# Kernel optimization log

Hardware: AMD Instinct MI355X
Metric: run time of the kernel (lower is better)

Reference implementation:

```python
import jax, jax.numpy as jnp
import numpy as np

H, D = 8, 32
IN, HID, OUT = 256, 256, 128
N_PAR, N_FIG, N_TAB, N_CIT = 100000, 20000, 20000, 50000
E = 200000


def setup_inputs() -> dict:
    key = jax.random.key(0)
    ks = iter(jax.random.split(key, 80))
    def nrm(shape, s=0.05):
        return jax.random.normal(next(ks), shape, dtype=jnp.float32) * s
    def ridx(n):
        return jax.random.randint(next(ks), (E,), 0, n, dtype=jnp.int32)
    inp = {
        'x_par': nrm((N_PAR, IN), 1.0), 'x_fig': nrm((N_FIG, IN), 1.0),
        'x_tab': nrm((N_TAB, IN), 1.0), 'x_cit': nrm((N_CIT, IN), 1.0),
    }
    for t in ['par', 'fig', 'tab', 'cit']:
        inp[f'Wp_{t}'] = nrm((IN, HID)); inp[f'bp_{t}'] = nrm((HID,))
    for et in ['pf', 'fp', 'pt', 'tp', 'pc', 'cp']:
        inp[f'a_{et}_s'] = nrm((H, D)); inp[f'a_{et}_d'] = nrm((H, D))
    inp['k_w'] = nrm((HID, HID)); inp['k_b'] = nrm((HID,)); inp['q'] = nrm((HID,))
    for t in ['par', 'fig', 'tab', 'cit']:
        inp[f'Wh_{t}'] = nrm((HID, OUT)); inp[f'bh_{t}'] = nrm((OUT,))
    inp['cls_w'] = nrm((2 * OUT, 1)); inp['cls_b'] = nrm((1,))
    inp['pf_src'] = ridx(N_PAR); inp['pf_dst'] = ridx(N_FIG)
    inp['fp_src'] = ridx(N_FIG); inp['fp_dst'] = ridx(N_PAR)
    inp['pt_src'] = ridx(N_PAR); inp['pt_dst'] = ridx(N_TAB)
    inp['tp_src'] = ridx(N_TAB); inp['tp_dst'] = ridx(N_PAR)
    inp['pc_src'] = ridx(N_PAR); inp['pc_dst'] = ridx(N_CIT)
    inp['cp_src'] = ridx(N_CIT); inp['cp_dst'] = ridx(N_PAR)
    inp['target_node_idx'] = 5
    return inp


def _agg(xs, xd, si, di, a_s, a_d, n_dst):
    # HANConv metapath aggregation: GAT-style attention + per-dst softmax + scatter-sum + relu
    as_ = jnp.einsum('nhd,hd->nh', xs, a_s)            # [Ns,H]
    ad_ = jnp.einsum('nhd,hd->nh', xd, a_d)            # [Nd,H]
    alpha = jax.nn.leaky_relu(as_[si] + ad_[di], 0.2)  # [E,H]
    m = jax.ops.segment_max(alpha, di, num_segments=n_dst)
    m = jnp.where(jnp.isfinite(m), m, 0.0)
    ex = jnp.exp(alpha - m[di])
    den = jax.ops.segment_sum(ex, di, num_segments=n_dst)
    w = ex / (den[di] + 1e-16)
    out = jax.ops.segment_sum(xs[si] * w[:, :, None], di, num_segments=n_dst)  # [Nd,H,D]
    return jax.nn.relu(out.reshape(n_dst, H * D))


def _group(outs, q, kw, kb):
    # HANConv semantic (metapath-level) attention
    st = jnp.stack(outs)                               # [M,N,F]
    kmean = jnp.tanh(st @ kw + kb).mean(axis=1)        # [M,F]
    attn = jax.nn.softmax(kmean @ q)                   # [M]
    return jnp.einsum('m,mnf->nf', attn, st)


def reference(x_par, x_fig, x_tab, x_cit,
              Wp_par, bp_par, Wp_fig, bp_fig, Wp_tab, bp_tab, Wp_cit, bp_cit,
              a_pf_s, a_pf_d, a_fp_s, a_fp_d, a_pt_s, a_pt_d,
              a_tp_s, a_tp_d, a_pc_s, a_pc_d, a_cp_s, a_cp_d,
              k_w, k_b, q,
              Wh_par, bh_par, Wh_fig, bh_fig, Wh_tab, bh_tab, Wh_cit, bh_cit,
              cls_w, cls_b,
              pf_src, pf_dst, fp_src, fp_dst, pt_src, pt_dst,
              tp_src, tp_dst, pc_src, pc_dst, cp_src, cp_dst,
              target_node_idx):
    # per-node-type input projection
    h_par = (x_par @ Wp_par + bp_par).reshape(-1, H, D)
    h_fig = (x_fig @ Wp_fig + bp_fig).reshape(-1, H, D)
    h_tab = (x_tab @ Wp_tab + bp_tab).reshape(-1, H, D)
    h_cit = (x_cit @ Wp_cit + bp_cit).reshape(-1, H, D)
    # per-metapath message passing, grouped per destination node type
    o_fig = _group([_agg(h_par, h_fig, pf_src, pf_dst, a_pf_s, a_pf_d, N_FIG)], q, k_w, k_b)
    o_tab = _group([_agg(h_par, h_tab, pt_src, pt_dst, a_pt_s, a_pt_d, N_TAB)], q, k_w, k_b)
    o_cit = _group([_agg(h_par, h_cit, pc_src, pc_dst, a_pc_s, a_pc_d, N_CIT)], q, k_w, k_b)
    o_par = _group([
        _agg(h_fig, h_par, fp_src, fp_dst, a_fp_s, a_fp_d, N_PAR),
        _agg(h_tab, h_par, tp_src, tp_dst, a_tp_s, a_tp_d, N_PAR),
        _agg(h_cit, h_par, cp_src, cp_dst, a_cp_s, a_cp_d, N_PAR),
    ], q, k_w, k_b)
    # output heads (table/cited_paper heads computed in the original but unused for scores)
    par_emb = o_par @ Wh_par + bh_par
    fig_emb = o_fig @ Wh_fig + bh_fig
    _ = o_tab @ Wh_tab + bh_tab
    _ = o_cit @ Wh_cit + bh_cit
    # pairwise classifier: target figure embedding broadcast against every paragraph
    target = fig_emb[target_node_idx]
    comb = jnp.concatenate(
        [jnp.broadcast_to(target[None, :], (par_emb.shape[0], OUT)), par_emb], axis=1)
    scores = (comb @ cls_w + cls_b)[:, 0]
    return scores
```

## Files before the change

### kernel.cpp

```cpp
#include <hip/hip_runtime.h>
#include <hip/hip_bf16.h>
#include <math.h>

typedef float f32x4 __attribute__((ext_vector_type(4)));
typedef short bf16x8 __attribute__((ext_vector_type(8)));

#define NPAR 100000
#define NFIG 20000
#define NTAB 20000
#define NCIT 50000
#define NEDGE 200000
#define CAP 32
#define PFCAP 79

__device__ __forceinline__ unsigned short f2b(float f) {
    union { float f; unsigned u; } x; x.f = f;
    unsigned r = x.u + 0x7FFFu + ((x.u >> 16) & 1u);
    return (unsigned short)(r >> 16);
}
__device__ __forceinline__ float b2f(unsigned short b) {
    union { unsigned u; float f; } x; x.u = ((unsigned)b) << 16; return x.f;
}
__device__ __forceinline__ float fast_tanh(float x) {
    float e = __expf(2.f * x);
    return 1.f - 2.f * __builtin_amdgcn_rcpf(e + 1.f);
}
__device__ __forceinline__ void async_copy16(const unsigned short* g, unsigned short* l) {
    __builtin_amdgcn_global_load_lds(
        (const __attribute__((address_space(1))) unsigned int*)g,
        (__attribute__((address_space(3))) unsigned int*)l, 16, 0, 0);
}

__global__ void k_transpose5(const float* __restrict__ W0, const float* __restrict__ W1,
                             const float* __restrict__ W2, const float* __restrict__ W3,
                             const float* __restrict__ W4, unsigned short* __restrict__ WT) {
    int b = blockIdx.x, which = b >> 8, k = b & 255, n = threadIdx.x;
    const float* W = which == 0 ? W0 : which == 1 ? W1 : which == 2 ? W2 : which == 3 ? W3 : W4;
    WT[(size_t)which * 65536 + n * 256 + k] = f2b(W[k * 256 + n]);
}

__global__ void k_precompute(const float* __restrict__ WhF, const float* __restrict__ bhF,
                             const float* __restrict__ WhP, const float* __restrict__ bhP,
                             const float* __restrict__ clsw, const float* __restrict__ clsb,
                             float* __restrict__ u, float* __restrict__ v, float* __restrict__ smallb) {
    int t = threadIdx.x;
    float su = 0.f, sv = 0.f;
    for (int j = 0; j < 128; ++j) {
        su += WhF[t * 128 + j] * clsw[j];
        sv += WhP[t * 128 + j] * clsw[128 + j];
    }
    u[t] = su; v[t] = sv;
    if (t == 0) {
        float c = clsb[0];
        for (int j = 0; j < 128; ++j) c += bhF[j] * clsw[j] + bhP[j] * clsw[128 + j];
        smallb[264] = c;
    }
}

__global__ void k_edges(const int* __restrict__ d0, const int* __restrict__ d1,
                        const int* __restrict__ d2, int* __restrict__ count,
                        int* __restrict__ elist,
                        const int* __restrict__ psrc, const int* __restrict__ pdst,
                        const int* __restrict__ tgtp, int* __restrict__ mlist) {
    int b = blockIdx.x;
    int m = b / 782;
    int e = (b - m * 782) * 256 + threadIdx.x;
    if (e >= NEDGE) return;
    if (m < 3) {
        const int* dst = m == 0 ? d0 : m == 1 ? d1 : d2;
        int d = dst[e];
        int* cnt = count + (size_t)m * NPAR;
        int* el = elist + (size_t)m * NPAR * CAP;
        int slot = atomicAdd(&cnt[d], 1);
        if (slot < CAP) el[(size_t)d * CAP + slot] = e;
    } else {
        if (pdst[e] == tgtp[0]) {
            int slot = atomicAdd(&mlist[0], 1);
            if (slot < PFCAP) mlist[1 + slot] = psrc[e];
        }
    }
}

struct ProjPack {
    const float* X[4];
    const unsigned short* WT[4];
    const float* bias[4];
    unsigned short* H[4];
    const float* av[16];
    float* ov[16];
    int nrows[4];
    int bbase[4];
    int nv[4];
};

#define LOADA(k0, A0, A1) do { \
    const float4* _p = reinterpret_cast<const float4*>(Arow + (k0)); \
    A0 = _p[0]; A1 = _p[1]; } while (0)
#define WRITEA(buf, A0, A1) do { \
    __align__(16) unsigned short _t[8]; \
    _t[0] = f2b(A0.x); _t[1] = f2b(A0.y); _t[2] = f2b(A0.z); _t[3] = f2b(A0.w); \
    _t[4] = f2b(A1.x); _t[5] = f2b(A1.y); _t[6] = f2b(A1.z); _t[7] = f2b(A1.w); \
    *reinterpret_cast<uint4*>(&As[buf][arow * 32 + acol]) = *reinterpret_cast<const uint4*>(_t); } while (0)

__global__ __launch_bounds__(512, 4) void k_gemm_proj(ProjPack p) {
    __shared__ __align__(16) unsigned short As[2][128 * 32];
    __shared__ __align__(16) unsigned short Bs[2][256 * 32];
    int bid = blockIdx.x;
    int ty = (bid >= p.bbase[1]) + (bid >= p.bbase[2]) + (bid >= p.bbase[3]);
    int m0 = (bid - p.bbase[ty]) * 128;
    const float* Xf = p.X[ty];
    const unsigned short* B = p.WT[ty];
    unsigned short* Hout = p.H[ty];
    int Nrows = p.nrows[ty];
    int nv = p.nv[ty];

    int t = threadIdx.x, l = t & 63, w = t >> 6;
    int wm = (w >> 2) * 64, wn = (w & 3) * 64;
    int lr = l & 15, hi = l >> 4;
    int arow = t >> 2, acol = (t & 3) * 8;
    int arow_c = m0 + arow; if (arow_c > Nrows - 1) arow_c = Nrows - 1;
    const float* Arow = Xf + (size_t)arow_c * 256 + acol;
    f32x4 acc[4][4] = {};
    float4 aP0, aP1, aQ0, aQ1;

    auto stageB = [&](int buf, int k0) {
#pragma unroll
        for (int i = 0; i < 2; ++i) {
            int rowb = w * 32 + i * 16;
            async_copy16(B + (size_t)(rowb + (l >> 2)) * 256 + k0 + (l & 3) * 8,
                         &Bs[buf][rowb * 32]);
        }
    };

    LOADA(0, aP0, aP1);
    stageB(0, 0);
    WRITEA(0, aP0, aP1);
    LOADA(32, aQ0, aQ1);
    asm volatile("s_waitcnt vmcnt(2) lgkmcnt(0)" ::: "memory");
    __builtin_amdgcn_s_barrier();

#pragma unroll
    for (int ks = 0; ks < 8; ++ks) {
        int cur = ks & 1;
        if (ks < 7) stageB(cur ^ 1, (ks + 1) * 32);
        if (ks < 6) {
            if ((ks & 1) == 0) LOADA((ks + 2) * 32, aP0, aP1);
            else               LOADA((ks + 2) * 32, aQ0, aQ1);
        }
        bf16x8 af[4], bfr[4];
#pragma unroll
        for (int mm = 0; mm < 4; ++mm)
            af[mm] = *reinterpret_cast<const bf16x8*>(&As[cur][(wm + mm * 16 + lr) * 32 + hi * 8]);
#pragma unroll
        for (int nn = 0; nn < 4; ++nn)
            bfr[nn] = *reinterpret_cast<const bf16x8*>(&Bs[cur][(wn + nn * 16 + lr) * 32 + hi * 8]);
#pragma unroll
        for (int mm = 0; mm < 4; ++mm)
#pragma unroll
            for (int nn = 0; nn < 4; ++nn)
                acc[mm][nn] = __builtin_amdgcn_mfma_f32_16x16x32_bf16(bfr[nn], af[mm], acc[mm][nn], 0, 0, 0);
        if (ks < 7) {
            if ((ks & 1) == 0) WRITEA(cur ^ 1, aQ0, aQ1);
            else               WRITEA(cur ^ 1, aP0, aP1);
            if (ks < 6) asm volatile("s_waitcnt vmcnt(2) lgkmcnt(0)" ::: "memory");
            else        asm volatile("s_waitcnt vmcnt(0) lgkmcnt(0)" ::: "memory");
            __builtin_amdgcn_s_barrier();
        }
    }

    __syncthreads();
    float* sattp = (float*)&As[0][0];
    unsigned short* Hst = &Bs[0][0];

    float4 bv4[4], av4[4][4];
#pragma unroll
    for (int nn = 0; nn < 4; ++nn)
        bv4[nn] = *reinterpret_cast<const float4*>(p.bias[ty] + wn + nn * 16 + hi * 4);
#pragma unroll
    for (int v = 0; v < 4; ++v)
        if (v < nv) {
            const float* A = p.av[ty * 4 + v];
#pragma unroll
            for (int nn = 0; nn < 4; ++nn)
                av4[v][nn] = *reinterpret_cast<const float4*>(A + wn + nn * 16 + hi * 4);
        }
    int h0 = (w & 3) * 2;
#pragma unroll
    for (int mm = 0; mm < 4; ++mm) {
        int lrow = wm + mm * 16 + lr;
        float sv[4][2] = {};
#pragma unroll
        for (int nn = 0; nn < 4; ++nn) {
            float c0 = acc[mm][nn][0] + bv4[nn].x;
            float c1 = acc[mm][nn][1] + bv4[nn].y;
            float c2 = acc[mm][nn][2] + bv4[nn].z;
            float c3 = acc[mm][nn][3] + bv4[nn].w;
#pragma unroll
            for (int v = 0; v < 4; ++v)
                if (v < nv)
                    sv[v][nn >> 1] += c0 * av4[v][nn].x + c1 * av4[v][nn].y +
                                      c2 * av4[v][nn].z + c3 * av4[v][nn].w;
        }
#pragma unroll
        for (int v = 0; v < 4; ++v)
            if (v < nv) {
#pragma unroll
                for (int hp = 0; hp < 2; ++hp) {
                    float s = sv[v][hp];
                    s += __shfl_xor(s, 16); s += __shfl_xor(s, 32);
                    if (hi == 0) sattp[v * 1024 + lrow * 8 + h0 + hp] = s;
                }
            }
    }

    if (ty != 0) {
        for (int hf = 0; hf < 2; ++hf) {
            if ((w >> 2) == hf) {
#pragma unroll
                for (int mm = 0; mm < 4; ++mm) {
                    int lr2 = mm * 16 + lr;
                    int swz = (lr2 & 7) << 4;
#pragma unroll
                    for (int nn = 0; nn < 4; ++nn) {
                        int colb = (wn + nn * 16 + hi * 4) * 2;
                        ushort4 o;
                        o.x = f2b(acc[mm][nn][0] + bv4[nn].x);
                        o.y = f2b(acc[mm][nn][1] + bv4[nn].y);
                        o.z = f2b(acc[mm][nn][2] + bv4[nn].z);
                        o.w = f2b(acc[mm][nn][3] + bv4[nn].w);
                        *reinterpret_cast<ushort4*>((char*)Hst + lr2 * 512 + (colb ^ swz)) = o;
                    }
                }
            }
            __syncthreads();
            {
                int row = t >> 3;
                int g = m0 + hf * 64 + row;
                if (g < Nrows) {
                    int swz = (row & 7) << 4;
#pragma unroll
                    for (int pass = 0; pass < 4; ++pass) {
                        int c = (t & 7) + pass * 8;
                        uint4 val = *reinterpret_cast<const uint4*>(
                            (const char*)Hst + row * 512 + ((c * 16) ^ swz));
                        *reinterpret_cast<uint4*>(Hout + (size_t)g * 256 + c * 8) = val;
                    }
                }
            }
            __syncthreads();
        }
    } else {
        __syncthreads();
    }

    for (int i = t; i < nv * 1024; i += 512) {
        int v = i >> 10, rem = i & 1023, lrow = rem >> 3, hd = rem & 7;
        int g = m0 + lrow;
        if (g < Nrows) p.ov[ty * 4 + v][(size_t)g * 8 + hd] = sattp[v * 1024 + lrow * 8 + hd];
    }
}

__global__ void k_pf_proj(const int* __restrict__ mlist, const float* __restrict__ Xp,
                          const unsigned short* __restrict__ WTp, const float* __restrict__ bp,
                          unsigned short* __restrict__ Hs) {
    int b = blockIdx.x;
    int cnt = mlist[0]; if (cnt > PFCAP) cnt = PFCAP;
    if (b >= cnt) return;
    int s = mlist[1 + b];
    __shared__ float xr[256];
    int t = threadIdx.x;
    xr[t] = Xp[(size_t)s * 256 + t];
    __syncthreads();
    const unsigned short* wrow = WTp + (size_t)t * 256;
    float acc = bp[t];
    for (int k = 0; k < 256; k += 8) {
        uint4 wv = *reinterpret_cast<const uint4*>(wrow + k);
        unsigned wsv[4] = { wv.x, wv.y, wv.z, wv.w };
#pragma unroll
        for (int j = 0; j < 4; ++j) {
            acc += xr[k + j * 2]     * b2f((unsigned short)(wsv[j] & 0xffffu));
            acc += xr[k + j * 2 + 1] * b2f((unsigned short)(wsv[j] >> 16));
        }
    }
    Hs[(size_t)b * 256 + t] = f2b(acc);
}

struct GKPack {
    const int* src[3]; const int* count[3]; const int* elist[3];
    const unsigned short* H[3]; const float* as_[3]; const float* ad_[3];
    const unsigned short* Bw; const float* kb; const float* v;
    float* ksum[3]; float* gout[3];
};
__global__ __launch_bounds__(512, 4) void k_gather_kmean(GKPack p) {
    __shared__ __align__(16) unsigned short Ar[3][32 * 256];
    __shared__ __align__(16) unsigned short Bs[2][256 * 32];
    int b2 = blockIdx.x;
    const unsigned short* Bw = p.Bw;
    int t = threadIdx.x, l = t & 63, w = t >> 6;
    int m0 = b2 * 32;
    int lg = l & 15, gb = l & 48;

    auto stageB = [&](int buf, int k0) {
#pragma unroll
        for (int i = 0; i < 2; ++i) {
            int rowb = w * 32 + i * 16;
            async_copy16(Bw + (size_t)(rowb + (l >> 2)) * 256 + k0 + (((l & 3) ^ ((l >> 2) & 3)) * 8),
                         &Bs[buf][rowb * 32]);
        }
    };
    stageB(0, 0);

    int ld = w * 4 + (l >> 4);
    int d = m0 + ld;

    float4 vv0 = *reinterpret_cast<const float4*>(p.v + lg * 16);
    float4 vv1 = *reinterpret_cast<const float4*>(p.v + lg * 16 + 4);
    float4 vv2 = *reinterpret_cast<const float4*>(p.v + lg * 16 + 8);
    float4 vv3 = *reinterpret_cast<const float4*>(p.v + lg * 16 + 12);
    float vr[16] = { vv0.x, vv0.y, vv0.z, vv0.w, vv1.x, vv1.y, vv1.z, vv1.w,
                     vv2.x, vv2.y, vv2.z, vv2.w, vv3.x, vv3.y, vv3.z, vv3.w };

    for (int mp = 0; mp < 3; ++mp) {
        const int* src = p.src[mp];
        const unsigned short* Hsrc = p.H[mp];
        const float* as_ = p.as_[mp];
        int cnt = p.count[mp][d]; if (cnt > CAP) cnt = CAP;
        int e1 = (lg < cnt) ? p.elist[mp][(size_t)d * CAP + lg] : -1;
        int e2 = (lg + 16 < cnt) ? p.elist[mp][(size_t)d * CAP + lg + 16] : -1;
        int s1 = (e1 >= 0) ? src[e1] : 0;
        int s2 = (e2 >= 0) ? src[e2] : 0;
        float adh = p.ad_[mp][d * 8 + (lg >> 1)];

        float ar[16];
#pragma unroll
        for (int k = 0; k < 16; ++k) ar[k] = 0.f;
        float den = 0.f;
        int sC = __shfl(s1, gb);
        const uint4* hp0 = reinterpret_cast<const uint4*>(Hsrc + (size_t)sC * 256 + lg * 16);
        uint4 hA = {}, hB = {};
        float asv = 0.f;
        if (cnt > 0) { hA = hp0[0]; hB = hp0[1]; asv = as_[sC * 8 + (lg >> 1)]; }
        for (int i = 0; i < cnt; ++i) {
            int iN = i + 1;
            uint4 nA = {}, nB = {};
            float nas = 0.f;
            if (iN < cnt) {
                int sN = (iN < 16) ? __shfl(s1, gb + (iN & 15)) : __shfl(s2, gb + ((iN - 16) & 15));
                const uint4* np = reinterpret_cast<const uint4*>(Hsrc + (size_t)sN * 256 + lg * 16);
                nA = np[0]; nB = np[1];
                nas = as_[sN * 8 + (lg >> 1)];
            }
            float al = asv + adh;
            al = al > 0.f ? al : 0.2f * al;
            float ex = __expf(al); den += ex;
            unsigned wds[8] = { hA.x, hA.y, hA.z, hA.w, hB.x, hB.y, hB.z, hB.w };
#pragma unroll
            for (int k = 0; k < 8; ++k) {
                ar[k * 2]     += ex * b2f((unsigned short)(wds[k] & 0xffffu));
                ar[k * 2 + 1] += ex * b2f((unsigned short)(wds[k] >> 16));
            }
            hA = nA; hB = nB; asv = nas;
        }
        float inv = 1.f / (den + 1e-16f);
        float gs = 0.f;
        __align__(16) unsigned short ob[16];
#pragma unroll
        for (int k = 0; k < 16; ++k) {
            float r = fmaxf(ar[k] * inv, 0.f);
            gs += r * vr[k];
            ob[k] = f2b(r);
        }
        int u0 = (lg * 2) ^ (ld & 7), u1 = (lg * 2 + 1) ^ (ld & 7);
        *reinterpret_cast<uint4*>(&Ar[mp][ld * 256 + u0 * 8]) = *reinterpret_cast<const uint4*>(ob);
        *reinterpret_cast<uint4*>(&Ar[mp][ld * 256 + u1 * 8]) = *reinterpret_cast<const uint4*>(ob + 8);
        gs += __shfl_xor(gs, 1); gs += __shfl_xor(gs, 2); gs += __shfl_xor(gs, 4); gs += __shfl_xor(gs, 8);
        if (lg == 0) p.gout[mp][d] = gs;
    }
    __syncthreads();

    int wm = (w >> 2) * 16, wn = (w & 3) * 64, lr = l & 15, hi = l >> 4;
    f32x4 acc0[4] = {}, acc1[4] = {}, acc2[4] = {};
#pragma unroll
    for (int ks = 0; ks < 8; ++ks) {
        int cur = ks & 1;
        if (ks < 7) stageB(cur ^ 1, (ks + 1) * 32);
        int rr = wm + lr;
        int aoff = rr * 256 + (((ks * 4 + hi) ^ (rr & 7)) * 8);
        bf16x8 a0 = *reinterpret_cast<const bf16x8*>(&Ar[0][aoff]);
        bf16x8 a1 = *reinterpret_cast<const bf16x8*>(&Ar[1][aoff]);
        bf16x8 a2 = *reinterpret_cast<const bf16x8*>(&Ar[2][aoff]);
        bf16x8 bfr[4];
#pragma unroll
        for (int nn = 0; nn < 4; ++nn) {
            int row = wn + nn * 16 + lr;
            bfr[nn] = *reinterpret_cast<const bf16x8*>(&Bs[cur][row * 32 + ((hi ^ (row & 3)) * 8)]);
        }
#pragma unroll
        for (int nn = 0; nn < 4; ++nn) {
            acc0[nn] = __builtin_amdgcn_mfma_f32_16x16x32_bf16(a0, bfr[nn], acc0[nn], 0, 0, 0);
            acc1[nn] = __builtin_amdgcn_mfma_f32_16x16x32_bf16(a1, bfr[nn], acc1[nn], 0, 0, 0);
            acc2[nn] = __builtin_amdgcn_mfma_f32_16x16x32_bf16(a2, bfr[nn], acc2[nn], 0, 0, 0);
        }
        if (ks < 7) {
            asm volatile("s_waitcnt vmcnt(0)" ::: "memory");
            __builtin_amdgcn_s_barrier();
        }
    }
#pragma unroll
    for (int nn = 0; nn < 4; ++nn) {
        int col = wn + nn * 16 + lr;
        float kbv = p.kb[col];
        float cs0 = 0.f, cs1 = 0.f, cs2 = 0.f;
#pragma unroll
        for (int r = 0; r < 4; ++r) {
            cs0 += fast_tanh(acc0[nn][r] + kbv);
            cs1 += fast_tanh(acc1[nn][r] + kbv);
            cs2 += fast_tanh(acc2[nn][r] + kbv);
        }
        cs0 += __shfl_xor(cs0, 16); cs0 += __shfl_xor(cs0, 32);
        cs1 += __shfl_xor(cs1, 16); cs1 += __shfl_xor(cs1, 32);
        cs2 += __shfl_xor(cs2, 16); cs2 += __shfl_xor(cs2, 32);
        if (hi == 0) {
            int rep = (b2 & 7) * 256 + col;
            atomicAdd(&p.ksum[0][rep], cs0);
            atomicAdd(&p.ksum[1][rep], cs1);
            atomicAdd(&p.ksum[2][rep], cs2);
        }
    }
}

__global__ void k_pf_acc(const int* __restrict__ mlist, const int* __restrict__ tgtp,
                         const unsigned short* __restrict__ Hs,
                         const float* __restrict__ as_pf, const float* __restrict__ ad_pf,
                         float* __restrict__ smallb) {
    __shared__ float sacc[4][256];
    __shared__ float sden[4][8];
    int t = threadIdx.x, w = t >> 6, l = t & 63;
    int tgt = tgtp[0];
    int cnt = mlist[0]; if (cnt > PFCAP) cnt = PFCAP;
    int h = l >> 3;
    float adh = ad_pf[tgt * 8 + h];
    float a0 = 0.f, a1 = 0.f, a2 = 0.f, a3 = 0.f, den = 0.f;
    for (int i = w; i < cnt; i += 4) {
        int s = mlist[1 + i];
        float al = as_pf[s * 8 + h] + adh;
        al = al > 0.f ? al : 0.2f * al;
        float ex = __expf(al);
        ushort4 hv = *reinterpret_cast<const ushort4*>(&Hs[(size_t)i * 256 + l * 4]);
        a0 += ex * b2f(hv.x); a1 += ex * b2f(hv.y); a2 += ex * b2f(hv.z); a3 += ex * b2f(hv.w);
        den += ex;
    }
    sacc[w][l * 4 + 0] = a0; sacc[w][l * 4 + 1] = a1;
    sacc[w][l * 4 + 2] = a2; sacc[w][l * 4 + 3] = a3;
    if ((l & 7) == 0) sden[w][h] = den;
    __syncthreads();
    smallb[t] = sacc[0][t] + sacc[1][t] + sacc[2][t] + sacc[3][t];
    if (t < 8) smallb[256 + t] = sden[0][t] + sden[1][t] + sden[2][t] + sden[3][t];
}

__global__ void k_finalize(const float* __restrict__ kacc, const float* __restrict__ q,
                           const float* __restrict__ u, float* __restrict__ smallb) {
    __shared__ float red[256];
    __shared__ float sm[3];
    int t = threadIdx.x;
    float qv = q[t];
    for (int m = 0; m < 3; ++m) {
        float acc = 0.f;
#pragma unroll
        for (int rep = 0; rep < 8; ++rep) acc += kacc[m * 2048 + rep * 256 + t];
        red[t] = acc * qv;
        __syncthreads();
        for (int s = 128; s > 0; s >>= 1) { if (t < s) red[t] += red[t + s]; __syncthreads(); }
        if (t == 0) sm[m] = red[0] / (float)NPAR;
        __syncthreads();
    }
    float den = smallb[256 + (t >> 5)];
    float rt = fmaxf(smallb[t] / (den + 1e-16f), 0.f);
    red[t] = rt * u[t];
    __syncthreads();
    for (int s = 128; s > 0; s >>= 1) { if (t < s) red[t] += red[t + s]; __syncthreads(); }
    if (t == 0) {
        float mx = fmaxf(sm[0], fmaxf(sm[1], sm[2]));
        float e0 = expf(sm[0] - mx), e1 = expf(sm[1] - mx), e2 = expf(sm[2] - mx);
        float sd = e0 + e1 + e2;
        smallb[265] = e0 / sd; smallb[266] = e1 / sd; smallb[267] = e2 / sd;
        smallb[268] = red[0] + smallb[264];
    }
}

__global__ void k_scores(const float* __restrict__ g, const float* __restrict__ smallb,
                         float* __restrict__ out) {
    int i = blockIdx.x * 256 + threadIdx.x;
    if (i >= NPAR) return;
    out[i] = smallb[268] + smallb[265] * g[i] + smallb[266] * g[NPAR + i] + smallb[267] * g[2 * NPAR + i];
}

extern "C" void kernel_launch(void* const* d_in, const int* in_sizes, int n_in,
                              void* d_out, int out_size, void* d_ws, size_t ws_size,
                              hipStream_t stream) {
    char* base = (char*)d_ws;
    size_t off = 0;
    auto alloc = [&](size_t b) -> void* { void* p = base + off; off += (b + 255) & ~(size_t)255; return p; };

    unsigned short* Hsmall = (unsigned short*)alloc((size_t)PFCAP * 256 * 2);
    unsigned short* h_fig = (unsigned short*)alloc((size_t)NFIG * 256 * 2);
    unsigned short* h_tab = (unsigned short*)alloc((size_t)NTAB * 256 * 2);
    unsigned short* h_cit = (unsigned short*)alloc((size_t)NCIT * 256 * 2);
    unsigned short* WTall = (unsigned short*)alloc((size_t)5 * 65536 * 2);
    unsigned short* WT_par = WTall, *WT_fig = WTall + 65536, *WT_tab = WTall + 2 * 65536,
                  *WT_cit = WTall + 3 * 65536, *kwT = WTall + 4 * 65536;
    float* as_pf = (float*)alloc((size_t)NPAR * 8 * 4);
    float* ad_fp = (float*)alloc((size_t)NPAR * 8 * 4);
    float* ad_tp = (float*)alloc((size_t)NPAR * 8 * 4);
    float* ad_cp = (float*)alloc((size_t)NPAR * 8 * 4);
    float* as_fp = (float*)alloc((size_t)NFIG * 8 * 4);
    float* ad_pf = (float*)alloc((size_t)NFIG * 8 * 4);
    float* as_tp = (float*)alloc((size_t)NTAB * 8 * 4);
    float* as_cp = (float*)alloc((size_t)NCIT * 8 * 4);
    float* gbuf  = (float*)alloc((size_t)3 * NPAR * 4);
    int* count3  = (int*)alloc((size_t)3 * NPAR * 4);
    int* elist3  = (int*)alloc((size_t)3 * NPAR * CAP * 4);
    float* kacc  = (float*)alloc((size_t)3 * 8 * 256 * 4);
    float* smallb = (float*)alloc(512 * 4);
    int* mlist   = (int*)alloc((1 + PFCAP) * 4);
    float* uvec  = (float*)alloc(256 * 4);
    float* vvec  = (float*)alloc(256 * 4);

    hipMemsetAsync(kacc, 0, 24576 + 2048 + 512, stream);
    hipMemsetAsync(count3, 0, (size_t)3 * NPAR * 4, stream);

    k_transpose5<<<5 * 256, 256, 0, stream>>>((const float*)d_in[4], (const float*)d_in[6],
                                              (const float*)d_in[8], (const float*)d_in[10],
                                              (const float*)d_in[24], WTall);

    k_precompute<<<1, 256, 0, stream>>>((const float*)d_in[29], (const float*)d_in[30],
                                        (const float*)d_in[27], (const float*)d_in[28],
                                        (const float*)d_in[35], (const float*)d_in[36],
                                        uvec, vvec, smallb);

    k_edges<<<4 * 782, 256, 0, stream>>>((const int*)d_in[40], (const int*)d_in[44],
                                         (const int*)d_in[48], count3, elist3,
                                         (const int*)d_in[37], (const int*)d_in[38],
                                         (const int*)d_in[49], mlist);
    k_pf_proj<<<PFCAP, 256, 0, stream>>>(mlist, (const float*)d_in[0], WT_par,
                                         (const float*)d_in[5], Hsmall);

    ProjPack pp;
    pp.X[0] = (const float*)d_in[0]; pp.X[1] = (const float*)d_in[1];
    pp.X[2] = (const float*)d_in[2]; pp.X[3] = (const float*)d_in[3];
    pp.WT[0] = WT_par; pp.WT[1] = WT_fig; pp.WT[2] = WT_tab; pp.WT[3] = WT_cit;
    pp.bias[0] = (const float*)d_in[5]; pp.bias[1] = (const float*)d_in[7];
    pp.bias[2] = (const float*)d_in[9]; pp.bias[3] = (const float*)d_in[11];
    pp.H[0] = h_fig; pp.H[1] = h_fig; pp.H[2] = h_tab; pp.H[3] = h_cit;
    pp.nrows[0] = NPAR; pp.nrows[1] = NFIG; pp.nrows[2] = NTAB; pp.nrows[3] = NCIT;
    pp.bbase[0] = 0; pp.bbase[1] = 782; pp.bbase[2] = 939; pp.bbase[3] = 1096;
    pp.nv[0] = 4; pp.nv[1] = 2; pp.nv[2] = 1; pp.nv[3] = 1;
    for (int i = 0; i < 16; ++i) { pp.av[i] = nullptr; pp.ov[i] = nullptr; }
    pp.av[0] = (const float*)d_in[12]; pp.ov[0] = as_pf;
    pp.av[1] = (const float*)d_in[15]; pp.ov[1] = ad_fp;
    pp.av[2] = (const float*)d_in[19]; pp.ov[2] = ad_tp;
    pp.av[3] = (const float*)d_in[23]; pp.ov[3] = ad_cp;
    pp.av[4] = (const float*)d_in[14]; pp.ov[4] = as_fp;
    pp.av[5] = (const float*)d_in[13]; pp.ov[5] = ad_pf;
    pp.av[8] = (const float*)d_in[18]; pp.ov[8] = as_tp;
    pp.av[12] = (const float*)d_in[22]; pp.ov[12] = as_cp;
    k_gemm_proj<<<1487, 512, 0, stream>>>(pp);

    k_pf_acc<<<1, 256, 0, stream>>>(mlist, (const int*)d_in[49], Hsmall, as_pf, ad_pf, smallb);

    GKPack gk;
    gk.src[0] = (const int*)d_in[39]; gk.src[1] = (const int*)d_in[43]; gk.src[2] = (const int*)d_in[47];
    gk.count[0] = count3; gk.count[1] = count3 + NPAR; gk.count[2] = count3 + 2 * NPAR;
    gk.elist[0] = elist3; gk.elist[1] = elist3 + (size_t)NPAR * CAP; gk.elist[2] = elist3 + (size_t)2 * NPAR * CAP;
    gk.H[0] = h_fig; gk.H[1] = h_tab; gk.H[2] = h_cit;
    gk.as_[0] = as_fp; gk.as_[1] = as_tp; gk.as_[2] = as_cp;
    gk.ad_[0] = ad_fp; gk.ad_[1] = ad_tp; gk.ad_[2] = ad_cp;
    gk.Bw = kwT; gk.kb = (const float*)d_in[25]; gk.v = vvec;
    gk.ksum[0] = kacc; gk.ksum[1] = kacc + 2048; gk.ksum[2] = kacc + 4096;
    gk.gout[0] = gbuf; gk.gout[1] = gbuf + NPAR; gk.gout[2] = gbuf + 2 * NPAR;
    k_gather_kmean<<<3125, 512, 0, stream>>>(gk);

    k_finalize<<<1, 256, 0, stream>>>(kacc, (const float*)d_in[26], uvec, smallb);
    k_scores<<<391, 256, 0, stream>>>(gbuf, smallb, (float*)d_out);
}
```

Baseline: 339.5 us.

## Triple-buffer B tiles in projection GEMM and store source ids in edge lists

The projection GEMM moves from double to triple buffering of the B shared-memory tiles, so B loads are issued two k-steps ahead, and the wait counts are adjusted to match. Separately, the edge-bucketing kernel now stores each edge's source node id instead of its edge index. This removes one dependent indirect load per edge in the gather kernel. The cost is more LDS per block in the GEMM, which may reduce occupancy.

Measured after the change: 341.9 us. About the same (+0.7%).

```diff
diff --git a/kernel.cpp b/kernel.cpp
--- a/kernel.cpp
+++ b/kernel.cpp
@@ -58,8 +58,10 @@
 }
 
 __global__ void k_edges(const int* __restrict__ d0, const int* __restrict__ d1,
-                        const int* __restrict__ d2, int* __restrict__ count,
-                        int* __restrict__ elist,
+                        const int* __restrict__ d2,
+                        const int* __restrict__ s0, const int* __restrict__ s1,
+                        const int* __restrict__ s2,
+                        int* __restrict__ count, int* __restrict__ elist,
                         const int* __restrict__ psrc, const int* __restrict__ pdst,
                         const int* __restrict__ tgtp, int* __restrict__ mlist) {
     int b = blockIdx.x;
@@ -68,11 +70,12 @@
     if (e >= NEDGE) return;
     if (m < 3) {
         const int* dst = m == 0 ? d0 : m == 1 ? d1 : d2;
+        const int* src = m == 0 ? s0 : m == 1 ? s1 : s2;
         int d = dst[e];
         int* cnt = count + (size_t)m * NPAR;
         int* el = elist + (size_t)m * NPAR * CAP;
         int slot = atomicAdd(&cnt[d], 1);
-        if (slot < CAP) el[(size_t)d * CAP + slot] = e;
+        if (slot < CAP) el[(size_t)d * CAP + slot] = src[e];
     } else {
         if (pdst[e] == tgtp[0]) {
             int slot = atomicAdd(&mlist[0], 1);
@@ -104,7 +107,7 @@
 
 __global__ __launch_bounds__(512, 4) void k_gemm_proj(ProjPack p) {
     __shared__ __align__(16) unsigned short As[2][128 * 32];
-    __shared__ __align__(16) unsigned short Bs[2][256 * 32];
+    __shared__ __align__(16) unsigned short Bs[3][256 * 32];
     int bid = blockIdx.x;
     int ty = (bid >= p.bbase[1]) + (bid >= p.bbase[2]) + (bid >= p.bbase[3]);
     int m0 = (bid - p.bbase[ty]) * 128;
@@ -135,22 +138,23 @@
     LOADA(0, aP0, aP1);
     stageB(0, 0);
     WRITEA(0, aP0, aP1);
+    stageB(1, 32);
     LOADA(32, aQ0, aQ1);
-    asm volatile("s_waitcnt vmcnt(2) lgkmcnt(0)" ::: "memory");
+    asm volatile("s_waitcnt vmcnt(4) lgkmcnt(0)" ::: "memory");
     __builtin_amdgcn_s_barrier();
 
 #pragma unroll
     for (int ks = 0; ks < 8; ++ks) {
-        int cur = ks & 1;
-        if (ks < 7) stageB(cur ^ 1, (ks + 1) * 32);
+        int cur = ks % 3;
         if (ks < 6) {
+            stageB((ks + 2) % 3, (ks + 2) * 32);
             if ((ks & 1) == 0) LOADA((ks + 2) * 32, aP0, aP1);
             else               LOADA((ks + 2) * 32, aQ0, aQ1);
         }
         bf16x8 af[4], bfr[4];
 #pragma unroll
         for (int mm = 0; mm < 4; ++mm)
-            af[mm] = *reinterpret_cast<const bf16x8*>(&As[cur][(wm + mm * 16 + lr) * 32 + hi * 8]);
+            af[mm] = *reinterpret_cast<const bf16x8*>(&As[ks & 1][(wm + mm * 16 + lr) * 32 + hi * 8]);
 #pragma unroll
         for (int nn = 0; nn < 4; ++nn)
             bfr[nn] = *reinterpret_cast<const bf16x8*>(&Bs[cur][(wn + nn * 16 + lr) * 32 + hi * 8]);
@@ -160,9 +164,9 @@
             for (int nn = 0; nn < 4; ++nn)
                 acc[mm][nn] = __builtin_amdgcn_mfma_f32_16x16x32_bf16(bfr[nn], af[mm], acc[mm][nn], 0, 0, 0);
         if (ks < 7) {
-            if ((ks & 1) == 0) WRITEA(cur ^ 1, aQ0, aQ1);
-            else               WRITEA(cur ^ 1, aP0, aP1);
-            if (ks < 6) asm volatile("s_waitcnt vmcnt(2) lgkmcnt(0)" ::: "memory");
+            if ((ks & 1) == 0) WRITEA((ks & 1) ^ 1, aQ0, aQ1);
+            else               WRITEA((ks & 1) ^ 1, aP0, aP1);
+            if (ks < 6) asm volatile("s_waitcnt vmcnt(4) lgkmcnt(0)" ::: "memory");
             else        asm volatile("s_waitcnt vmcnt(0) lgkmcnt(0)" ::: "memory");
             __builtin_amdgcn_s_barrier();
         }
@@ -286,7 +290,7 @@
 }
 
 struct GKPack {
-    const int* src[3]; const int* count[3]; const int* elist[3];
+    const int* count[3]; const int* elist[3];
     const unsigned short* H[3]; const float* as_[3]; const float* ad_[3];
     const unsigned short* Bw; const float* kb; const float* v;
     float* ksum[3]; float* gout[3];
@@ -321,14 +325,11 @@
                      vv2.x, vv2.y, vv2.z, vv2.w, vv3.x, vv3.y, vv3.z, vv3.w };
 
     for (int mp = 0; mp < 3; ++mp) {
-        const int* src = p.src[mp];
         const unsigned short* Hsrc = p.H[mp];
         const float* as_ = p.as_[mp];
         int cnt = p.count[mp][d]; if (cnt > CAP) cnt = CAP;
-        int e1 = (lg < cnt) ? p.elist[mp][(size_t)d * CAP + lg] : -1;
-        int e2 = (lg + 16 < cnt) ? p.elist[mp][(size_t)d * CAP + lg + 16] : -1;
-        int s1 = (e1 >= 0) ? src[e1] : 0;
-        int s2 = (e2 >= 0) ? src[e2] : 0;
+        int s1 = (lg < cnt) ? p.elist[mp][(size_t)d * CAP + lg] : 0;
+        int s2 = (lg + 16 < cnt) ? p.elist[mp][(size_t)d * CAP + lg + 16] : 0;
         float adh = p.ad_[mp][d * 8 + (lg >> 1)];
 
         float ar[16];
@@ -539,7 +540,10 @@
                                         uvec, vvec, smallb);
 
     k_edges<<<4 * 782, 256, 0, stream>>>((const int*)d_in[40], (const int*)d_in[44],
-                                         (const int*)d_in[48], count3, elist3,
+                                         (const int*)d_in[48],
+                                         (const int*)d_in[39], (const int*)d_in[43],
+                                         (const int*)d_in[47],
+                                         count3, elist3,
                                          (const int*)d_in[37], (const int*)d_in[38],
                                          (const int*)d_in[49], mlist);
     k_pf_proj<<<PFCAP, 256, 0, stream>>>(mlist, (const float*)d_in[0], WT_par,
@@ -569,7 +573,6 @@
     k_pf_acc<<<1, 256, 0, stream>>>(mlist, (const int*)d_in[49], Hsmall, as_pf, ad_pf, smallb);
 
     GKPack gk;
-    gk.src[0] = (const int*)d_in[39]; gk.src[1] = (const int*)d_in[43]; gk.src[2] = (const int*)d_in[47];
     gk.count[0] = count3; gk.count[1] = count3 + NPAR; gk.count[2] = count3 + 2 * NPAR;
     gk.elist[0] = elist3; gk.elist[1] = elist3 + (size_t)NPAR * CAP; gk.elist[2] = elist3 + (size_t)2 * NPAR * CAP;
     gk.H[0] = h_fig; gk.H[1] = h_tab; gk.H[2] = h_cit;
```
